# Kernel tuning notes

Hardware: AMD Instinct MI355X
Metric: run time of the kernel (lower is better)

## Reference

```python
import jax, jax.numpy as jnp
import numpy as np

B, L, D, T = 32, 512, 1024, 256
MAX_MENTION_LEN = 10
NEG_INF = float('-inf')


def _static_bounds_and_keep():
    # Full (start, end) grid, flattened row-major like torch's .view(-1, 2)
    s = np.repeat(np.arange(L), L)
    e = np.tile(np.arange(L), L)
    bounds = np.stack([s, e], axis=-1)            # [L*L, 2]
    keep = (e - s) <= MAX_MENTION_LEN             # static per-position mask
    idx = np.nonzero(keep)[0]
    return jnp.asarray(bounds[keep], jnp.int32), jnp.asarray(idx, jnp.int32)


def setup_inputs() -> dict:
    key = jax.random.key(0)
    k0, k1, k2 = jax.random.split(key, 3)
    text_encodings = jax.random.normal(k0, (B, L, D), dtype=jnp.float32)
    mask_ctxt = jnp.ones((B, L), dtype=jnp.int32)
    # word -> wordpiece mapping: [start, end_exclusive); values kept in [1, L)
    tokens_mapping = jax.random.randint(k1, (B, T, 2), 1, L).astype(jnp.int32)
    W = jax.random.normal(k2, (D, 3), dtype=jnp.float32) * 0.02
    b = jnp.zeros((3,), dtype=jnp.float32)
    return {"text_encodings": text_encodings, "mask_ctxt": mask_ctxt,
            "tokens_mapping": tokens_mapping, "W": W, "b": b}


def reference(text_encodings, mask_ctxt, tokens_mapping, W, b):
    # per-token start / end / mention logits
    logits = jnp.einsum('bld,dk->blk', text_encodings, W) + b  # [B, L, 3]
    valid_tok = (mask_ctxt == 1)
    start_lp = jnp.where(valid_tok, logits[:, :, 0], NEG_INF)
    end_lp = jnp.where(valid_tok, logits[:, :, 1], NEG_INF)
    mention_lp = jnp.where(valid_tok, logits[:, :, 2], NEG_INF)

    # scores[b, s, e] = start[b, s] + end[b, e] + sum_{i=s..e} mention[b, i]
    scores = start_lp[:, :, None] + end_lp[:, None, :]          # [B, L, L]
    csum = jnp.cumsum(mention_lp, axis=1)                        # [B, L]
    csum_prev = jnp.concatenate(
        [jnp.zeros((csum.shape[0], 1), csum.dtype), csum[:, :-1]], axis=1)
    scores = scores + (csum[:, None, :] - csum_prev[:, :, None])

    # mention_sizes > 0  <=>  e >= s
    pos = jnp.arange(L)
    size_ok = pos[None, :, None] <= pos[None, None, :]           # [1, L, L]

    # token-boundary masks (scatter 1 at word starts / ends, zero col 0)
    bidx = jnp.arange(tokens_mapping.shape[0])[:, None]
    ts = jnp.zeros(mask_ctxt.shape, jnp.int32).at[bidx, tokens_mapping[:, :, 0]].set(1)
    ts = ts.at[:, 0].set(0)
    te = jnp.zeros(mask_ctxt.shape, jnp.int32).at[bidx, tokens_mapping[:, :, 1] - 1].set(1)
    te = te.at[:, 0].set(0)
    vse = ts[:, :, None] * te[:, None, :]                        # bmm outer product

    valid = size_ok & (mask_ctxt[:, :, None] > 0) & (vse > 0)
    scores = jnp.where(valid, scores, NEG_INF)

    scores_flat = scores.reshape(scores.shape[0], -1)            # [B, L*L]
    bounds_keep, keep_idx = _static_bounds_and_keep()
    out_scores = scores_flat[:, keep_idx]                        # [B, K]
    out_bounds = jnp.broadcast_to(bounds_keep[None],
                                  (scores.shape[0],) + bounds_keep.shape)
    return out_scores, out_bounds
```

## Files before the change

kernel.cpp:

```cpp
#include <hip/hip_runtime.h>
#include <math.h>

#define BB 32
#define LL 512
#define DD 1024
#define TT 256
#define NK 136393
#define NK_LIN 131273
#define S_LIN 502
#define NEG_BIG  -3.0e38f
#define NEG_MASK -1.0e30f
#define P_TOT (BB * NK)
#define SC4 (P_TOT / 4)
#define GEMV_BLOCKS (BB * LL / 4)
#define TAILQ_CNT (BB * 8)
#define MEMSET_CNT ((SC4 + 255) / 256)
#define BCHUNKS ((NK + 255) / 256)
#define D2_BLOCKS (TAILQ_CNT + MEMSET_CNT + 2 * BCHUNKS)

typedef float f4v __attribute__((ext_vector_type(4)));
typedef float f2v __attribute__((ext_vector_type(2)));

__device__ __forceinline__ int off_s(int s) {
    return (s <= S_LIN) ? s * (s + 21) / 2 : NK_LIN + (s - S_LIN) * LL;
}
__device__ __forceinline__ void invert(int k, int& s, int& e) {
    if (k >= NK_LIN) {
        const int r = k - NK_LIN;
        s = S_LIN + (r >> 9);
        e = r & 511;
    } else {
        float f = sqrtf(8.0f * (float)k + 441.0f);
        s = (int)((f - 21.0f) * 0.5f);
        if (s < 0) s = 0;
        if (s > 501) s = 501;
        while ((s + 1) * (s + 22) / 2 <= k) ++s;
        while (s * (s + 21) / 2 > k) --s;
        e = k - s * (s + 21) / 2;
    }
}

__global__ __launch_bounds__(256) void gemv_kernel(
    const float* __restrict__ text, const float* __restrict__ W,
    const float* __restrict__ bias, const int* __restrict__ mask,
    float* __restrict__ slp, float* __restrict__ elp, float* __restrict__ mlp)
{
    const int wid  = threadIdx.x >> 6;
    const int lane = threadIdx.x & 63;
    const int row  = blockIdx.x * 4 + wid;
    const f4v* t4 = (const f4v*)(text + (size_t)row * DD);
    const f4v* w4 = (const f4v*)W;
    float a0 = 0.f, a1 = 0.f, a2 = 0.f;
#pragma unroll
    for (int j = 0; j < 4; ++j) {
        const int fi = lane + j * 64;
        f4v v  = t4[fi];
        f4v w0 = w4[fi * 3 + 0];
        f4v w1 = w4[fi * 3 + 1];
        f4v w2 = w4[fi * 3 + 2];
        a0 += v.x * w0.x;  a1 += v.x * w0.y;  a2 += v.x * w0.z;
        a0 += v.y * w0.w;  a1 += v.y * w1.x;  a2 += v.y * w1.y;
        a0 += v.z * w1.z;  a1 += v.z * w1.w;  a2 += v.z * w2.x;
        a0 += v.w * w2.y;  a1 += v.w * w2.z;  a2 += v.w * w2.w;
    }
#pragma unroll
    for (int o = 32; o; o >>= 1) {
        a0 += __shfl_down(a0, o);
        a1 += __shfl_down(a1, o);
        a2 += __shfl_down(a2, o);
    }
    if (lane == 0) {
        const int m = mask[row];
        slp[row] = (m == 1) ? a0 + bias[0] : NEG_MASK;
        elp[row] = (m == 1) ? a1 + bias[1] : NEG_MASK;
        mlp[row] = (m == 1) ? a2 + bias[2] : NEG_MASK;
    }
}

__global__ __launch_bounds__(256) void emit_kernel(
    const float* __restrict__ slp, const float* __restrict__ elp,
    const float* __restrict__ mlp, const int* __restrict__ mask,
    const int* __restrict__ tmap, float* __restrict__ out)
{
    const int id = blockIdx.x;
    const int t  = threadIdx.x;

    if (id < TAILQ_CNT) {
        const int b  = id >> 3;
        const int r0 = (id & 7) << 6;
        __shared__ float sl[LL], el[LL], ml[LL];
        __shared__ unsigned char fsb[LL], feb[LL];
        const int base = b * LL;
        const int i0 = t, i1 = t + 256;
        const int mk0 = mask[base + i0], mk1 = mask[base + i1];
        sl[i0] = slp[base + i0]; el[i0] = elp[base + i0]; ml[i0] = mlp[base + i0];
        sl[i1] = slp[base + i1]; el[i1] = elp[base + i1]; ml[i1] = mlp[base + i1];
        fsb[i0] = 0; fsb[i1] = 0; feb[i0] = 0; feb[i1] = 0;
        __syncthreads();
        {
            int s0 = tmap[((size_t)b * TT + t) * 2 + 0];
            int e0 = tmap[((size_t)b * TT + t) * 2 + 1] - 1;
            s0 = min(max(s0, 0), LL - 1);
            e0 = min(max(e0, 0), LL - 1);
            fsb[s0] = 1;
            feb[e0] = 1;
        }
        __syncthreads();
        fsb[i0] = (i0 != 0 && fsb[i0] && mk0 == 1) ? 1 : 0;
        fsb[i1] = (fsb[i1] && mk1 == 1) ? 1 : 0;
        feb[i0] = (i0 != 0 && feb[i0]) ? 1 : 0;
        __syncthreads();

        for (int it = t; it < 64 * 5; it += 256) {
            const int s_loc = it / 5;
            const int slot  = it - s_loc * 5;
            const int s     = r0 + s_loc;
            const int offf  = b * NK + off_s(s);
            const int rowlen = (s <= S_LIN) ? (s + 11) : LL;
            const int p0 = ((((offf + s) >> 2) - 1 + slot) << 2);
            if (p0 < offf || p0 >= offf + rowlen) continue;
            float vals[4];
            bool nonpure = false;
#pragma unroll
            for (int kk = 0; kk < 4; ++kk) {
                const int p = p0 + kk;
                float v = NEG_BIG;
                int rr, er;
                if (p < offf + rowlen) { rr = s;     er = p - offf; }
                else                   { rr = s + 1; er = p - offf - rowlen; }
                if (rr < LL) {
                    if (er >= rr) {
                        nonpure = true;
                        if (fsb[rr] && feb[er]) {
                            float w = 0.f;
                            for (int l = rr; l <= er; ++l) w += ml[l];
                            v = sl[rr] + el[er] + w;
                            if (v < -1.0e29f) v = NEG_BIG;
                        }
                    }
                } else {
                    nonpure = true;
                }
                vals[kk] = v;
            }
            if (nonpure) {
                f4v vv = {vals[0], vals[1], vals[2], vals[3]};
                *(f4v*)(out + p0) = vv;
            }
        }
        return;
    }

    if (id < TAILQ_CNT + MEMSET_CNT) {
        const int gid = (id - TAILQ_CNT) * 256 + t;
        if (gid >= SC4) return;
        const int p4 = gid * 4;
        int b = p4 / NK;
        int k = p4 - b * NK;
        int s, e;
        invert(k, s, e);
        bool pure;
        if (e + 3 < s) {
            pure = true;
        } else {
            pure = true;
            int ss = s, ee = e;
            int rowlen = (ss <= S_LIN) ? (ss + 11) : LL;
#pragma unroll
            for (int kk = 0; kk < 4; ++kk) {
                if (ee >= ss) { pure = false; break; }
                ++ee;
                if (ee >= rowlen) {
                    ee = 0; ++ss;
                    if (ss >= LL) ss = 0;
                    rowlen = (ss <= S_LIN) ? (ss + 11) : LL;
                }
            }
        }
        if (pure) {
            f4v neg = {NEG_BIG, NEG_BIG, NEG_BIG, NEG_BIG};
            *(f4v*)(out + p4) = neg;
        }
        return;
    }

    const int q = id - TAILQ_CNT - MEMSET_CNT;
    const int g = (q >= BCHUNKS) ? 1 : 0;
    const int c = q - g * BCHUNKS;
    const int p = c * 256 + t;
    if (p >= NK) return;
    int s, e;
    invert(p, s, e);
    f2v v = {(float)s, (float)e};
    f2v* bp = (f2v*)(out + (size_t)P_TOT);
#pragma unroll
    for (int j = 0; j < 16; ++j) {
        const int b = g * 16 + j;
        bp[(size_t)b * NK + p] = v;
    }
}

extern "C" void kernel_launch(void* const* d_in, const int* in_sizes, int n_in,
                              void* d_out, int out_size, void* d_ws, size_t ws_size,
                              hipStream_t stream) {
    const float* text = (const float*)d_in[0];
    const int*   mask = (const int*)d_in[1];
    const int*   tmap = (const int*)d_in[2];
    const float* W    = (const float*)d_in[3];
    const float* bias = (const float*)d_in[4];
    float* out = (float*)d_out;

    float* slp = (float*)d_ws;
    float* elp = slp + (size_t)BB * LL;
    float* mlp = elp + (size_t)BB * LL;

    gemv_kernel<<<GEMV_BLOCKS, 256, 0, stream>>>(text, W, bias, mask,
                                                 slp, elp, mlp);
    emit_kernel<<<D2_BLOCKS, 256, 0, stream>>>(slp, elp, mlp, mask, tmap, out);
}
```

Before: 26.68 us.

## Move bounds writing into GEMV kernel and widen memset stores

Output-bounds generation moves out of the emit kernel into the GEMV kernel. Bounds blocks are interleaved one in nine with GEMV blocks, so the bandwidth-bound bounds stores overlap the compute-light GEMV, and they now write 16-byte vectors covering two pairs instead of 8-byte ones. The NEG fill in the emit kernel handles 16 floats per thread instead of 4, which cuts the number of blocks and the inversion cost. The risks are more complex alignment and edge handling for odd batches, and possible load imbalance between the mixed block types.

After: 35.64 us. +33.6%, slower.

```diff
diff --git a/kernel.cpp b/kernel.cpp
--- a/kernel.cpp
+++ b/kernel.cpp
@@ -12,11 +12,15 @@
 #define NEG_MASK -1.0e30f
 #define P_TOT (BB * NK)
 #define SC4 (P_TOT / 4)
+#define SC16 (P_TOT / 16)
 #define GEMV_BLOCKS (BB * LL / 4)
+#define NP2 ((NK + 1) / 2)
+#define BPG ((NP2 + 255) / 256)
+#define BND_BLOCKS (BPG * 2)
+#define GRID1 (512 * 9 + (BND_BLOCKS - 512))
+#define MS16_CNT ((SC16 + 255) / 256)
 #define TAILQ_CNT (BB * 8)
-#define MEMSET_CNT ((SC4 + 255) / 256)
-#define BCHUNKS ((NK + 255) / 256)
-#define D2_BLOCKS (TAILQ_CNT + MEMSET_CNT + 2 * BCHUNKS)
+#define GRID2 (MS16_CNT + TAILQ_CNT)
 
 typedef float f4v __attribute__((ext_vector_type(4)));
 typedef float f2v __attribute__((ext_vector_type(2)));
@@ -39,41 +43,100 @@
         e = k - s * (s + 21) / 2;
     }
 }
-
-__global__ __launch_bounds__(256) void gemv_kernel(
+__device__ __forceinline__ void adv(int& s, int& e) {
+    const int rowlen = (s <= S_LIN) ? (s + 11) : LL;
+    if (++e >= rowlen) { e = 0; ++s; }
+}
+
+__global__ __launch_bounds__(256) void gemv_bounds_kernel(
     const float* __restrict__ text, const float* __restrict__ W,
     const float* __restrict__ bias, const int* __restrict__ mask,
-    float* __restrict__ slp, float* __restrict__ elp, float* __restrict__ mlp)
+    float* __restrict__ slp, float* __restrict__ elp, float* __restrict__ mlp,
+    float* __restrict__ out)
 {
-    const int wid  = threadIdx.x >> 6;
-    const int lane = threadIdx.x & 63;
-    const int row  = blockIdx.x * 4 + wid;
-    const f4v* t4 = (const f4v*)(text + (size_t)row * DD);
-    const f4v* w4 = (const f4v*)W;
-    float a0 = 0.f, a1 = 0.f, a2 = 0.f;
-#pragma unroll
-    for (int j = 0; j < 4; ++j) {
-        const int fi = lane + j * 64;
-        f4v v  = t4[fi];
-        f4v w0 = w4[fi * 3 + 0];
-        f4v w1 = w4[fi * 3 + 1];
-        f4v w2 = w4[fi * 3 + 2];
-        a0 += v.x * w0.x;  a1 += v.x * w0.y;  a2 += v.x * w0.z;
-        a0 += v.y * w0.w;  a1 += v.y * w1.x;  a2 += v.y * w1.y;
-        a0 += v.z * w1.z;  a1 += v.z * w1.w;  a2 += v.z * w2.x;
-        a0 += v.w * w2.y;  a1 += v.w * w2.z;  a2 += v.w * w2.w;
-    }
-#pragma unroll
-    for (int o = 32; o; o >>= 1) {
-        a0 += __shfl_down(a0, o);
-        a1 += __shfl_down(a1, o);
-        a2 += __shfl_down(a2, o);
-    }
-    if (lane == 0) {
-        const int m = mask[row];
-        slp[row] = (m == 1) ? a0 + bias[0] : NEG_MASK;
-        elp[row] = (m == 1) ? a1 + bias[1] : NEG_MASK;
-        mlp[row] = (m == 1) ? a2 + bias[2] : NEG_MASK;
+    const int id = blockIdx.x;
+    const int t  = threadIdx.x;
+
+    int bv = -1;
+    int g  = -1;
+    if (id < 512 * 9) {
+        const int q = id / 9, r = id - q * 9;
+        if (r == 8) bv = q; else g = q * 8 + r;
+    } else {
+        bv = 512 + (id - 512 * 9);
+    }
+
+    if (g >= 0) {
+        const int wid  = t >> 6;
+        const int lane = t & 63;
+        const int row  = g * 4 + wid;
+        const f4v* t4 = (const f4v*)(text + (size_t)row * DD);
+        const f4v* w4 = (const f4v*)W;
+        float a0 = 0.f, a1 = 0.f, a2 = 0.f;
+#pragma unroll
+        for (int j = 0; j < 4; ++j) {
+            const int fi = lane + j * 64;
+            f4v v  = t4[fi];
+            f4v w0 = w4[fi * 3 + 0];
+            f4v w1 = w4[fi * 3 + 1];
+            f4v w2 = w4[fi * 3 + 2];
+            a0 += v.x * w0.x;  a1 += v.x * w0.y;  a2 += v.x * w0.z;
+            a0 += v.y * w0.w;  a1 += v.y * w1.x;  a2 += v.y * w1.y;
+            a0 += v.z * w1.z;  a1 += v.z * w1.w;  a2 += v.z * w2.x;
+            a0 += v.w * w2.y;  a1 += v.w * w2.z;  a2 += v.w * w2.w;
+        }
+#pragma unroll
+        for (int o = 32; o; o >>= 1) {
+            a0 += __shfl_down(a0, o);
+            a1 += __shfl_down(a1, o);
+            a2 += __shfl_down(a2, o);
+        }
+        if (lane == 0) {
+            const int m = mask[row];
+            slp[row] = (m == 1) ? a0 + bias[0] : NEG_MASK;
+            elp[row] = (m == 1) ? a1 + bias[1] : NEG_MASK;
+            mlp[row] = (m == 1) ? a2 + bias[2] : NEG_MASK;
+        }
+        return;
+    }
+
+    const int gg = (bv >= BPG) ? 1 : 0;
+    const int c  = bv - gg * BPG;
+    const int pp = c * 256 + t;
+    if (pp >= NP2) return;
+    const int p0 = 2 * pp;
+    int s0, e0; invert(p0, s0, e0);
+    int s1 = s0, e1 = e0; adv(s1, e1);
+    int s2 = s1, e2 = e1; if (p0 + 2 < NK) adv(s2, e2);
+    const float S0 = (float)s0, E0 = (float)e0;
+    const float S1 = (float)s1, E1 = (float)e1;
+    const float S2 = (float)s2, E2 = (float)e2;
+    float* bp = out + (size_t)P_TOT;
+#pragma unroll
+    for (int j = 0; j < 16; ++j) {
+        const int bb = gg * 16 + j;
+        const size_t B = (size_t)bb * NK;
+        if ((bb & 1) == 0) {
+            if (p0 + 1 < NK) {
+                f4v vv = {S0, E0, S1, E1};
+                *(f4v*)(bp + (B + p0) * 2) = vv;
+            } else {
+                f2v v2 = {S0, E0};
+                *(f2v*)(bp + (B + p0) * 2) = v2;
+            }
+        } else {
+            if (pp == 0) {
+                f2v v2 = {0.f, 0.f};
+                *(f2v*)(bp + B * 2) = v2;
+            }
+            if (p0 + 2 < NK) {
+                f4v vv = {S1, E1, S2, E2};
+                *(f4v*)(bp + (B + p0 + 1) * 2) = vv;
+            } else if (p0 + 1 < NK) {
+                f2v v2 = {S1, E1};
+                *(f2v*)(bp + (B + p0 + 1) * 2) = v2;
+            }
+        }
     }
 }
 
@@ -85,90 +148,28 @@
     const int id = blockIdx.x;
     const int t  = threadIdx.x;
 
-    if (id < TAILQ_CNT) {
-        const int b  = id >> 3;
-        const int r0 = (id & 7) << 6;
-        __shared__ float sl[LL], el[LL], ml[LL];
-        __shared__ unsigned char fsb[LL], feb[LL];
-        const int base = b * LL;
-        const int i0 = t, i1 = t + 256;
-        const int mk0 = mask[base + i0], mk1 = mask[base + i1];
-        sl[i0] = slp[base + i0]; el[i0] = elp[base + i0]; ml[i0] = mlp[base + i0];
-        sl[i1] = slp[base + i1]; el[i1] = elp[base + i1]; ml[i1] = mlp[base + i1];
-        fsb[i0] = 0; fsb[i1] = 0; feb[i0] = 0; feb[i1] = 0;
-        __syncthreads();
-        {
-            int s0 = tmap[((size_t)b * TT + t) * 2 + 0];
-            int e0 = tmap[((size_t)b * TT + t) * 2 + 1] - 1;
-            s0 = min(max(s0, 0), LL - 1);
-            e0 = min(max(e0, 0), LL - 1);
-            fsb[s0] = 1;
-            feb[e0] = 1;
-        }
-        __syncthreads();
-        fsb[i0] = (i0 != 0 && fsb[i0] && mk0 == 1) ? 1 : 0;
-        fsb[i1] = (fsb[i1] && mk1 == 1) ? 1 : 0;
-        feb[i0] = (i0 != 0 && feb[i0]) ? 1 : 0;
-        __syncthreads();
-
-        for (int it = t; it < 64 * 5; it += 256) {
-            const int s_loc = it / 5;
-            const int slot  = it - s_loc * 5;
-            const int s     = r0 + s_loc;
-            const int offf  = b * NK + off_s(s);
-            const int rowlen = (s <= S_LIN) ? (s + 11) : LL;
-            const int p0 = ((((offf + s) >> 2) - 1 + slot) << 2);
-            if (p0 < offf || p0 >= offf + rowlen) continue;
-            float vals[4];
-            bool nonpure = false;
-#pragma unroll
-            for (int kk = 0; kk < 4; ++kk) {
-                const int p = p0 + kk;
-                float v = NEG_BIG;
-                int rr, er;
-                if (p < offf + rowlen) { rr = s;     er = p - offf; }
-                else                   { rr = s + 1; er = p - offf - rowlen; }
-                if (rr < LL) {
-                    if (er >= rr) {
-                        nonpure = true;
-                        if (fsb[rr] && feb[er]) {
-                            float w = 0.f;
-                            for (int l = rr; l <= er; ++l) w += ml[l];
-                            v = sl[rr] + el[er] + w;
-                            if (v < -1.0e29f) v = NEG_BIG;
-                        }
-                    }
-                } else {
-                    nonpure = true;
-                }
-                vals[kk] = v;
-            }
-            if (nonpure) {
-                f4v vv = {vals[0], vals[1], vals[2], vals[3]};
-                *(f4v*)(out + p0) = vv;
-            }
-        }
-        return;
-    }
-
-    if (id < TAILQ_CNT + MEMSET_CNT) {
-        const int gid = (id - TAILQ_CNT) * 256 + t;
-        if (gid >= SC4) return;
-        const int p4 = gid * 4;
-        int b = p4 / NK;
-        int k = p4 - b * NK;
+    if (id < MS16_CNT) {
+        const int gid = id * 256 + t;
+        if (gid >= SC16) return;
+        const int p16 = gid * 16;
+        const int b = p16 / NK;
+        const int k = p16 - b * NK;
         int s, e;
         invert(k, s, e);
-        bool pure;
-        if (e + 3 < s) {
-            pure = true;
-        } else {
-            pure = true;
-            int ss = s, ee = e;
-            int rowlen = (ss <= S_LIN) ? (ss + 11) : LL;
+        const f4v neg = {NEG_BIG, NEG_BIG, NEG_BIG, NEG_BIG};
+        if (e + 15 < s) {
+            f4v* q = (f4v*)(out + p16);
+            q[0] = neg; q[1] = neg; q[2] = neg; q[3] = neg;
+            return;
+        }
+        int ss = s, ee = e;
+        int rowlen = (ss <= S_LIN) ? (ss + 11) : LL;
+#pragma unroll
+        for (int qq = 0; qq < 4; ++qq) {
+            bool pure = true;
 #pragma unroll
             for (int kk = 0; kk < 4; ++kk) {
-                if (ee >= ss) { pure = false; break; }
+                if (ee >= ss) pure = false;
                 ++ee;
                 if (ee >= rowlen) {
                     ee = 0; ++ss;
@@ -176,27 +177,73 @@
                     rowlen = (ss <= S_LIN) ? (ss + 11) : LL;
                 }
             }
-        }
-        if (pure) {
-            f4v neg = {NEG_BIG, NEG_BIG, NEG_BIG, NEG_BIG};
-            *(f4v*)(out + p4) = neg;
+            if (pure) *(f4v*)(out + p16 + 4 * qq) = neg;
         }
         return;
     }
 
-    const int q = id - TAILQ_CNT - MEMSET_CNT;
-    const int g = (q >= BCHUNKS) ? 1 : 0;
-    const int c = q - g * BCHUNKS;
-    const int p = c * 256 + t;
-    if (p >= NK) return;
-    int s, e;
-    invert(p, s, e);
-    f2v v = {(float)s, (float)e};
-    f2v* bp = (f2v*)(out + (size_t)P_TOT);
-#pragma unroll
-    for (int j = 0; j < 16; ++j) {
-        const int b = g * 16 + j;
-        bp[(size_t)b * NK + p] = v;
+    const int tq = id - MS16_CNT;
+    const int b  = tq >> 3;
+    const int r0 = (tq & 7) << 6;
+    __shared__ float sl[LL], el[LL], ml[LL];
+    __shared__ unsigned char fsb[LL], feb[LL];
+    const int base = b * LL;
+    const int i0 = t, i1 = t + 256;
+    const int mk0 = mask[base + i0], mk1 = mask[base + i1];
+    sl[i0] = slp[base + i0]; el[i0] = elp[base + i0]; ml[i0] = mlp[base + i0];
+    sl[i1] = slp[base + i1]; el[i1] = elp[base + i1]; ml[i1] = mlp[base + i1];
+    fsb[i0] = 0; fsb[i1] = 0; feb[i0] = 0; feb[i1] = 0;
+    __syncthreads();
+    {
+        int s0 = tmap[((size_t)b * TT + t) * 2 + 0];
+        int e0 = tmap[((size_t)b * TT + t) * 2 + 1] - 1;
+        s0 = min(max(s0, 0), LL - 1);
+        e0 = min(max(e0, 0), LL - 1);
+        fsb[s0] = 1;
+        feb[e0] = 1;
+    }
+    __syncthreads();
+    fsb[i0] = (i0 != 0 && fsb[i0] && mk0 == 1) ? 1 : 0;
+    fsb[i1] = (fsb[i1] && mk1 == 1) ? 1 : 0;
+    feb[i0] = (i0 != 0 && feb[i0]) ? 1 : 0;
+    __syncthreads();
+
+    for (int it = t; it < 64 * 5; it += 256) {
+        const int s_loc = it / 5;
+        const int slot  = it - s_loc * 5;
+        const int s     = r0 + s_loc;
+        const int offf  = b * NK + off_s(s);
+        const int rowlen = (s <= S_LIN) ? (s + 11) : LL;
+        const int p0 = ((((offf + s) >> 2) - 1 + slot) << 2);
+        if (p0 < offf || p0 >= offf + rowlen) continue;
+        float vals[4];
+        bool nonpure = false;
+#pragma unroll
+        for (int kk = 0; kk < 4; ++kk) {
+            const int p = p0 + kk;
+            float v = NEG_BIG;
+            int rr, er;
+            if (p < offf + rowlen) { rr = s;     er = p - offf; }
+            else                   { rr = s + 1; er = p - offf - rowlen; }
+            if (rr < LL) {
+                if (er >= rr) {
+                    nonpure = true;
+                    if (fsb[rr] && feb[er]) {
+                        float w = 0.f;
+                        for (int l = rr; l <= er; ++l) w += ml[l];
+                        v = sl[rr] + el[er] + w;
+                        if (v < -1.0e29f) v = NEG_BIG;
+                    }
+                }
+            } else {
+                nonpure = true;
+            }
+            vals[kk] = v;
+        }
+        if (nonpure) {
+            f4v vv = {vals[0], vals[1], vals[2], vals[3]};
+            *(f4v*)(out + p0) = vv;
+        }
     }
 }
 
@@ -214,7 +261,7 @@
     float* elp = slp + (size_t)BB * LL;
     float* mlp = elp + (size_t)BB * LL;
 
-    gemv_kernel<<<GEMV_BLOCKS, 256, 0, stream>>>(text, W, bias, mask,
-                                                 slp, elp, mlp);
-    emit_kernel<<<D2_BLOCKS, 256, 0, stream>>>(slp, elp, mlp, mask, tmap, out);
-}
+    gemv_bounds_kernel<<<GRID1, 256, 0, stream>>>(text, W, bias, mask,
+                                                  slp, elp, mlp, out);
+    emit_kernel<<<GRID2, 256, 0, stream>>>(slp, elp, mlp, mask, tmap, out);
+}
```
